# Kernel optimization log

Hardware: AMD Instinct MI355X
Metric: run time of the kernel (lower is better)

Reference implementation:

```python
import jax, jax.numpy as jnp
import numpy as np

B, S, E, D, DV = 4, 4096, 1024, 64, 1024
NEG_INF = jnp.inf


def setup_inputs() -> dict:
    key = jax.random.key(0)
    ks = jax.random.split(key, 5)
    x = jax.random.normal(ks[0], (B, S, E), dtype=jnp.float32)
    Wq = jax.random.normal(ks[1], (E, D), dtype=jnp.float32) * 0.02
    Wk = jax.random.normal(ks[2], (E, D), dtype=jnp.float32) * 0.02
    Wv = jax.random.normal(ks[3], (E, DV), dtype=jnp.float32) * 0.02
    bq = jnp.zeros((D,), dtype=jnp.float32)
    bk = jnp.zeros((D,), dtype=jnp.float32)
    bv = jnp.zeros((DV,), dtype=jnp.float32)
    pad = jax.random.uniform(ks[4], (B, S)) > 0.9
    mask_padding_x = jnp.where(pad, -jnp.inf, 0.0).astype(jnp.float32)
    return {"x": x, "Wq": Wq, "bq": bq, "Wk": Wk, "bk": bk,
            "Wv": Wv, "bv": bv, "mask_padding_x": mask_padding_x}


def _padding_mask(mask_padding_x):
    # Faithful replication of the torch mask-combination logic (self-attn: y mask == x mask).
    mask_x = mask_padding_x[:, :, None]   # [B, Sx, 1]
    mask_y = mask_padding_x[:, None, :]   # [B, 1, Sy]
    # (-inf)*(-inf)=+inf kept; 0*(-inf)=nan -> 0
    prod = jnp.nan_to_num(mask_x * mask_y, nan=0.0, posinf=jnp.inf)
    # one side padded -> -inf; both padded -> inf + (-inf) + (-inf) = nan -> 0; both valid -> 0
    final = jnp.nan_to_num(prod + mask_y + mask_x, nan=0.0, posinf=0.0, neginf=-jnp.inf)
    return final  # [B, Sx, Sy]


def _causal_mask(n):
    # create_mask: strictly-upper-triangular -inf, zeros on/below diagonal
    return jnp.triu(jnp.full((n, n), -jnp.inf, dtype=jnp.float32), k=1)


def reference(x, Wq, bq, Wk, bk, Wv, bv, mask_padding_x):
    # self-attention path (y = x), mask=True (causal), dropout in eval mode (identity)
    Q = jnp.einsum('bse,ed->bsd', x, Wq) + bq          # [B,S,D]
    K = jnp.einsum('bse,ed->bsd', x, Wk) + bk          # [B,S,D]
    V = jnp.einsum('bse,ev->bsv', x, Wv) + bv          # [B,S,DV]
    scale = 1.0 / jnp.sqrt(jnp.float32(D))
    QK = jnp.einsum('bqd,bkd->bqk', Q, K) * scale      # [B,S,S]
    QK = QK + _padding_mask(mask_padding_x)
    QK = QK + _causal_mask(x.shape[1])
    attn = jax.nn.softmax(QK, axis=-1)
    return jnp.einsum('bqk,bkv->bqv', attn, V)         # [B,S,DV]
```

## Files before the change

### kernel.cpp

```cpp
#include <hip/hip_runtime.h>
#include <stdint.h>

typedef __attribute__((ext_vector_type(8))) short short8;
typedef __attribute__((ext_vector_type(4))) float floatx4;

__device__ __forceinline__ unsigned short f2bf(float f) {
    unsigned u = __float_as_uint(f);
    u += 0x7FFFu + ((u >> 16) & 1u);
    return (unsigned short)(u >> 16);
}

__device__ __forceinline__ void gload_lds16(const void* g, void* l) {
    __builtin_amdgcn_global_load_lds(
        (const __attribute__((address_space(1))) unsigned int*)g,
        (__attribute__((address_space(3))) unsigned int*)l, 16, 0, 0);
}

__global__ __launch_bounds__(256)
void conv_x(const float* __restrict__ x, unsigned short* __restrict__ xb) {
    const size_t total = (size_t)16384 * 1024;
    for (size_t i = ((size_t)blockIdx.x * 256 + threadIdx.x) * 8; i < total;
         i += (size_t)2048 * 256 * 8) {
        float4 a = *(const float4*)&x[i];
        float4 b = *(const float4*)&x[i + 4];
        uint4 o;
        o.x = f2bf(a.x) | ((unsigned)f2bf(a.y) << 16);
        o.y = f2bf(a.z) | ((unsigned)f2bf(a.w) << 16);
        o.z = f2bf(b.x) | ((unsigned)f2bf(b.y) << 16);
        o.w = f2bf(b.z) | ((unsigned)f2bf(b.w) << 16);
        *(uint4*)&xb[i] = o;
    }
}

__global__ __launch_bounds__(256)
void transpose_w(const float* __restrict__ src, unsigned short* __restrict__ dst, int N) {
    __shared__ float T[64][65];
    const int t = threadIdx.x;
    const int k0 = blockIdx.x * 64, n0 = blockIdx.y * 64;
    const int r = t >> 4, c4 = (t & 15) * 4;
#pragma unroll
    for (int i = 0; i < 4; i++) {
        float4 v = *(const float4*)&src[(size_t)(k0 + r + 16 * i) * N + n0 + c4];
        T[r + 16 * i][c4] = v.x; T[r + 16 * i][c4 + 1] = v.y;
        T[r + 16 * i][c4 + 2] = v.z; T[r + 16 * i][c4 + 3] = v.w;
    }
    __syncthreads();
#pragma unroll
    for (int i = 0; i < 4; i++) {
        const int n = n0 + r + 16 * i;
        unsigned short b0 = f2bf(T[c4 + 0][r + 16 * i]);
        unsigned short b1 = f2bf(T[c4 + 1][r + 16 * i]);
        unsigned short b2 = f2bf(T[c4 + 2][r + 16 * i]);
        unsigned short b3 = f2bf(T[c4 + 3][r + 16 * i]);
        uint2 pv;
        pv.x = b0 | ((unsigned)b1 << 16);
        pv.y = b2 | ((unsigned)b3 << 16);
        *(uint2*)&dst[(size_t)n * 1024 + k0 + c4] = pv;
    }
}

__global__ __launch_bounds__(128)
void pack_bias(const float* __restrict__ bq, const float* __restrict__ bk,
               float* __restrict__ bqk) {
    const int t = threadIdx.x;
    bqk[t] = (t < 64) ? bq[t] : bk[t - 64];
}

template<bool TRS>
__global__ __launch_bounds__(256)
void gemm_bf16(const unsigned short* __restrict__ A,
               const unsigned short* __restrict__ Bt,
               const float* __restrict__ bias,
               unsigned short* __restrict__ out, int M, int N)
{
    __shared__ unsigned short As[128 * 32];
    __shared__ unsigned short Bs[128 * 32];
    const int tid = threadIdx.x;
    const int w = tid >> 6, l = tid & 63;
    const int quad = l >> 4, l16 = l & 15;
    const int wr = w >> 1, wc = w & 1;
    const int m0 = blockIdx.x * 128, n0 = blockIdx.y * 128;

    const int lr = l >> 2, lk = (l & 3) * 8;
    const unsigned short* Ag0 = A + (size_t)(m0 + w * 16 + lr) * 1024 + lk;
    const unsigned short* Ag1 = Ag0 + (size_t)64 * 1024;
    const unsigned short* Bg0 = Bt + (size_t)(n0 + w * 16 + lr) * 1024 + lk;
    const unsigned short* Bg1 = Bg0 + (size_t)64 * 1024;
    unsigned short* Al0 = &As[w * 512 + l * 8];
    unsigned short* Bl0 = &Bs[w * 512 + l * 8];

    floatx4 acc[4][4];
#pragma unroll
    for (int i = 0; i < 4; i++)
#pragma unroll
        for (int j = 0; j < 4; j++) acc[i][j] = (floatx4)0.f;

    for (int e0 = 0; e0 < 1024; e0 += 32) {
        gload_lds16(Ag0 + e0, Al0);
        gload_lds16(Ag1 + e0, Al0 + 2048);
        gload_lds16(Bg0 + e0, Bl0);
        gload_lds16(Bg1 + e0, Bl0 + 2048);
        __syncthreads();
        short8 af[4], bf[4];
#pragma unroll
        for (int i = 0; i < 4; i++)
            af[i] = *(const short8*)&As[(wr * 64 + i * 16 + l16) * 32 + quad * 8];
#pragma unroll
        for (int j = 0; j < 4; j++)
            bf[j] = *(const short8*)&Bs[(wc * 64 + j * 16 + l16) * 32 + quad * 8];
#pragma unroll
        for (int i = 0; i < 4; i++)
#pragma unroll
            for (int j = 0; j < 4; j++)
                acc[i][j] = __builtin_amdgcn_mfma_f32_16x16x32_bf16(af[i], bf[j], acc[i][j], 0, 0, 0);
        __syncthreads();
    }

#pragma unroll
    for (int j = 0; j < 4; j++) {
        const int n = n0 + wc * 64 + j * 16 + l16;
        const float bn = bias[n];
#pragma unroll
        for (int i = 0; i < 4; i++) {
            const int mb = m0 + wr * 64 + i * 16 + quad * 4;
            if (TRS) {
                unsigned short t[4];
#pragma unroll
                for (int r = 0; r < 4; r++) t[r] = f2bf(acc[i][j][r] + bn);
                uint2 pv;
                pv.x = t[0] | ((unsigned)t[1] << 16);
                pv.y = t[2] | ((unsigned)t[3] << 16);
                *(uint2*)&out[(size_t)n * M + mb] = pv;
            } else {
#pragma unroll
                for (int r = 0; r < 4; r++)
                    out[(size_t)(mb + r) * N + n] = f2bf(acc[i][j][r] + bn);
            }
        }
    }
}

__global__ __launch_bounds__(512, 4)
void attn_fused(const unsigned short* __restrict__ QKb,
                const unsigned short* __restrict__ Vt,
                const float* __restrict__ maskx,
                float* __restrict__ out)
{
    __shared__ unsigned short Qs[64 * 72];
    __shared__ unsigned short Ps[2][64 * 40];
    __shared__ float Ls[64];

    const int tid = threadIdx.x;
    const int wave = tid >> 6, lane = tid & 63;
    const int quad = lane >> 4, l16 = lane & 15;
    const int bid = blockIdx.x;
    const int dvh = bid & 1;
    const int b = (bid >> 1) & 3;
    const int t = bid >> 3;
    const int qt = (t < 32) ? (63 - t) : (t - 32);
    const int q0 = qt * 64;
    const int gq0 = b * 4096 + q0;

    if (tid < 64) Ls[tid] = 0.f;
    {
        const int r = tid >> 3, c = (tid & 7) * 8;
        uint4 v = *(const uint4*)&QKb[(size_t)(gq0 + r) * 128 + c];
        *(uint4*)&Qs[r * 72 + c] = v;
    }
    __syncthreads();

    const int rb = wave >> 1;
    const int kb = wave & 1;
    bool pq[4];
#pragma unroll
    for (int r = 0; r < 4; r++)
        pq[r] = maskx[b * 4096 + q0 + rb * 16 + quad * 4 + r] < -1e30f;

    const short8 qa0 = *(const short8*)&Qs[(rb * 16 + l16) * 72 + quad * 8];
    const short8 qa1 = *(const short8*)&Qs[(rb * 16 + l16) * 72 + 32 + quad * 8];

    floatx4 acc[4][4];
#pragma unroll
    for (int i = 0; i < 4; i++)
#pragma unroll
        for (int j = 0; j < 4; j++) acc[i][j] = (floatx4)0.f;
    float lacc[4] = {0.f, 0.f, 0.f, 0.f};

    const int niter = 2 * qt + 2;
    const float scale = 0.125f;
    const int dv0 = dvh * 512 + wave * 64;

    const unsigned short* kptr = QKb + ((size_t)(b * 4096 + kb * 16 + l16) * 128 + 64 + quad * 8);
    const float* mptr = maskx + b * 4096 + kb * 16 + l16;
    size_t voff[4];
#pragma unroll
    for (int cb = 0; cb < 4; cb++)
        voff[cb] = (size_t)(dv0 + cb * 16 + l16) * 16384 + b * 4096 + quad * 8;

    short8 kc0 = *(const short8*)kptr;
    short8 kc1 = *(const short8*)(kptr + 32);
    float mval = *mptr;

    for (int kt = 0; kt < niter; kt++) {
        const int k0 = kt * 32;
        short8 vb[4];
#pragma unroll
        for (int cb = 0; cb < 4; cb++)
            vb[cb] = *(const short8*)&Vt[voff[cb] + k0];
        floatx4 s = (floatx4)0.f;
        s = __builtin_amdgcn_mfma_f32_16x16x32_bf16(qa0, kc0, s, 0, 0, 0);
        s = __builtin_amdgcn_mfma_f32_16x16x32_bf16(qa1, kc1, s, 0, 0, 0);
        const bool pk = mval < -1e30f;
        {
            int kn = k0 + 32 + kb * 16 + l16;
            if (kn > 4095) kn = 4095;
            const unsigned short* np = QKb + ((size_t)(b * 4096 + kn) * 128 + 64 + quad * 8);
            kc0 = *(const short8*)np;
            kc1 = *(const short8*)(np + 32);
            mval = maskx[b * 4096 + kn];
        }
        const int kg = k0 + kb * 16 + l16;
        unsigned short pbits[4];
#pragma unroll
        for (int r = 0; r < 4; r++) {
            const int qrow = q0 + rb * 16 + quad * 4 + r;
            float p = 0.f;
            if (kg <= qrow && pk == pq[r]) p = __expf(s[r] * scale);
            lacc[r] += p;
            pbits[r] = f2bf(p);
        }
        unsigned short* Pw = Ps[kt & 1];
#pragma unroll
        for (int r = 0; r < 4; r++)
            Pw[(rb * 16 + quad * 4 + r) * 40 + kb * 16 + l16] = pbits[r];
        asm volatile("s_waitcnt lgkmcnt(0)" ::: "memory");
        __builtin_amdgcn_s_barrier();
        __builtin_amdgcn_sched_barrier(0);
        const unsigned short* Pr = Ps[kt & 1];
        short8 pa[4];
#pragma unroll
        for (int r2 = 0; r2 < 4; r2++)
            pa[r2] = *(const short8*)&Pr[(r2 * 16 + l16) * 40 + quad * 8];
#pragma unroll
        for (int cb = 0; cb < 4; cb++)
#pragma unroll
            for (int r2 = 0; r2 < 4; r2++)
                acc[r2][cb] = __builtin_amdgcn_mfma_f32_16x16x32_bf16(pa[r2], vb[cb], acc[r2][cb], 0, 0, 0);
    }

#pragma unroll
    for (int r = 0; r < 4; r++) {
        float v = lacc[r];
        v += __shfl_xor(v, 1);
        v += __shfl_xor(v, 2);
        v += __shfl_xor(v, 4);
        v += __shfl_xor(v, 8);
        if (l16 == 0) atomicAdd(&Ls[rb * 16 + quad * 4 + r], v);
    }
    __syncthreads();

#pragma unroll
    for (int r2 = 0; r2 < 4; r2++) {
#pragma unroll
        for (int r = 0; r < 4; r++) {
            const int qrow = q0 + r2 * 16 + quad * 4 + r;
            const float inv = 1.f / Ls[r2 * 16 + quad * 4 + r];
#pragma unroll
            for (int cb = 0; cb < 4; cb++)
                out[(size_t)(b * 4096 + qrow) * 1024 + dv0 + cb * 16 + l16] = acc[r2][cb][r] * inv;
        }
    }
}

extern "C" void kernel_launch(void* const* d_in, const int* in_sizes, int n_in,
                              void* d_out, int out_size, void* d_ws, size_t ws_size,
                              hipStream_t stream) {
    const float* x  = (const float*)d_in[0];
    const float* Wq = (const float*)d_in[1];
    const float* bq = (const float*)d_in[2];
    const float* Wk = (const float*)d_in[3];
    const float* bk = (const float*)d_in[4];
    const float* Wv = (const float*)d_in[5];
    const float* bv = (const float*)d_in[6];
    const float* mk = (const float*)d_in[7];
    float* out = (float*)d_out;

    const int M = 4 * 4096;
    char* ws = (char*)d_ws;
    unsigned short* Xb   = (unsigned short*)ws;
    unsigned short* Vt   = (unsigned short*)(ws + (33554432));
    unsigned short* Wvt  = (unsigned short*)(ws + (67108864));
    unsigned short* Wqkt = (unsigned short*)(ws + (69206016));
    unsigned short* QKb  = (unsigned short*)(ws + (69468160));
    float*          bqk  = (float*)(ws + (73662464));

    conv_x<<<2048, 256, 0, stream>>>(x, Xb);
    transpose_w<<<dim3(16, 16), 256, 0, stream>>>(Wv, Wvt, 1024);
    transpose_w<<<dim3(16, 1), 256, 0, stream>>>(Wq, Wqkt, 64);
    transpose_w<<<dim3(16, 1), 256, 0, stream>>>(Wk, Wqkt + 64 * 1024, 64);
    pack_bias<<<1, 128, 0, stream>>>(bq, bk, bqk);

    gemm_bf16<true ><<<dim3(128, 8), 256, 0, stream>>>(Xb, Wvt, bv, Vt, M, 1024);
    gemm_bf16<false><<<dim3(128, 1), 256, 0, stream>>>(Xb, Wqkt, bqk, QKb, M, 128);

    attn_fused<<<dim3(4 * 64 * 2), 512, 0, stream>>>(QKb, Vt, mk, out);
}
```

Measured before the change: 417.3 us.

## Split attention work into 256-thread blocks over eight DV slices

The fused attention kernel now uses 256-thread blocks, each covering 128 of the 1024 value columns instead of 512, so the grid grows from 512 to 2048 blocks. Each wave now computes scores for two 16-row query slabs and accumulates two 16-column value tiles instead of four. This gives more, smaller blocks for load balancing and occupancy across CUs. The cost is that QK^T scores and the exp/softmax numerators are recomputed four times as often, once per DV slice.

```diff
diff --git a/kernel.cpp b/kernel.cpp
--- a/kernel.cpp
+++ b/kernel.cpp
@@ -140,7 +140,7 @@
     }
 }
 
-__global__ __launch_bounds__(512, 4)
+__global__ __launch_bounds__(256, 4)
 void attn_fused(const unsigned short* __restrict__ QKb,
                 const unsigned short* __restrict__ Vt,
                 const float* __restrict__ maskx,
@@ -154,63 +154,80 @@
     const int wave = tid >> 6, lane = tid & 63;
     const int quad = lane >> 4, l16 = lane & 15;
     const int bid = blockIdx.x;
-    const int dvh = bid & 1;
+    const int dvl = bid & 1;
     const int b = (bid >> 1) & 3;
-    const int t = bid >> 3;
+    const int dvh2 = (bid >> 3) & 3;
+    const int t = bid >> 5;
+    const int dvq = dvh2 * 2 + dvl;
     const int qt = (t < 32) ? (63 - t) : (t - 32);
     const int q0 = qt * 64;
     const int gq0 = b * 4096 + q0;
 
     if (tid < 64) Ls[tid] = 0.f;
     {
-        const int r = tid >> 3, c = (tid & 7) * 8;
-        uint4 v = *(const uint4*)&QKb[(size_t)(gq0 + r) * 128 + c];
-        *(uint4*)&Qs[r * 72 + c] = v;
+#pragma unroll
+        for (int j = 0; j < 2; j++) {
+            const int c = tid + j * 256;
+            const int r = c >> 3, c8 = (c & 7) * 8;
+            uint4 v = *(const uint4*)&QKb[(size_t)(gq0 + r) * 128 + c8];
+            *(uint4*)&Qs[r * 72 + c8] = v;
+        }
     }
     __syncthreads();
 
-    const int rb = wave >> 1;
+    const int rbp = wave >> 1;
     const int kb = wave & 1;
-    bool pq[4];
-#pragma unroll
-    for (int r = 0; r < 4; r++)
-        pq[r] = maskx[b * 4096 + q0 + rb * 16 + quad * 4 + r] < -1e30f;
-
-    const short8 qa0 = *(const short8*)&Qs[(rb * 16 + l16) * 72 + quad * 8];
-    const short8 qa1 = *(const short8*)&Qs[(rb * 16 + l16) * 72 + 32 + quad * 8];
-
-    floatx4 acc[4][4];
+
+    unsigned pqm = 0;
+#pragma unroll
+    for (int h = 0; h < 2; h++)
+#pragma unroll
+        for (int r = 0; r < 4; r++)
+            if (maskx[b * 4096 + q0 + (rbp * 2 + h) * 16 + quad * 4 + r] < -1e30f)
+                pqm |= 1u << (h * 4 + r);
+
+    short8 qa[2][2];
+#pragma unroll
+    for (int h = 0; h < 2; h++) {
+        qa[h][0] = *(const short8*)&Qs[((rbp * 2 + h) * 16 + l16) * 72 + quad * 8];
+        qa[h][1] = *(const short8*)&Qs[((rbp * 2 + h) * 16 + l16) * 72 + 32 + quad * 8];
+    }
+
+    floatx4 acc[4][2];
 #pragma unroll
     for (int i = 0; i < 4; i++)
 #pragma unroll
-        for (int j = 0; j < 4; j++) acc[i][j] = (floatx4)0.f;
-    float lacc[4] = {0.f, 0.f, 0.f, 0.f};
+        for (int j = 0; j < 2; j++) acc[i][j] = (floatx4)0.f;
+    float lacc[2][4] = {{0.f, 0.f, 0.f, 0.f}, {0.f, 0.f, 0.f, 0.f}};
 
     const int niter = 2 * qt + 2;
     const float scale = 0.125f;
-    const int dv0 = dvh * 512 + wave * 64;
+    const int dv0 = dvq * 128 + wave * 32;
 
     const unsigned short* kptr = QKb + ((size_t)(b * 4096 + kb * 16 + l16) * 128 + 64 + quad * 8);
-    const float* mptr = maskx + b * 4096 + kb * 16 + l16;
-    size_t voff[4];
-#pragma unroll
-    for (int cb = 0; cb < 4; cb++)
+    size_t voff[2];
+#pragma unroll
+    for (int cb = 0; cb < 2; cb++)
         voff[cb] = (size_t)(dv0 + cb * 16 + l16) * 16384 + b * 4096 + quad * 8;
 
     short8 kc0 = *(const short8*)kptr;
     short8 kc1 = *(const short8*)(kptr + 32);
-    float mval = *mptr;
+    float mval = maskx[b * 4096 + kb * 16 + l16];
 
     for (int kt = 0; kt < niter; kt++) {
         const int k0 = kt * 32;
-        short8 vb[4];
-#pragma unroll
-        for (int cb = 0; cb < 4; cb++)
+        short8 vb[2];
+#pragma unroll
+        for (int cb = 0; cb < 2; cb++)
             vb[cb] = *(const short8*)&Vt[voff[cb] + k0];
-        floatx4 s = (floatx4)0.f;
-        s = __builtin_amdgcn_mfma_f32_16x16x32_bf16(qa0, kc0, s, 0, 0, 0);
-        s = __builtin_amdgcn_mfma_f32_16x16x32_bf16(qa1, kc1, s, 0, 0, 0);
-        const bool pk = mval < -1e30f;
+        floatx4 s[2];
+#pragma unroll
+        for (int h = 0; h < 2; h++) {
+            s[h] = (floatx4)0.f;
+            s[h] = __builtin_amdgcn_mfma_f32_16x16x32_bf16(qa[h][0], kc0, s[h], 0, 0, 0);
+            s[h] = __builtin_amdgcn_mfma_f32_16x16x32_bf16(qa[h][1], kc1, s[h], 0, 0, 0);
+        }
+        const unsigned pkb = (mval < -1e30f) ? 1u : 0u;
         {
             int kn = k0 + 32 + kb * 16 + l16;
             if (kn > 4095) kn = 4095;
@@ -220,19 +237,19 @@
             mval = maskx[b * 4096 + kn];
         }
         const int kg = k0 + kb * 16 + l16;
-        unsigned short pbits[4];
-#pragma unroll
-        for (int r = 0; r < 4; r++) {
-            const int qrow = q0 + rb * 16 + quad * 4 + r;
-            float p = 0.f;
-            if (kg <= qrow && pk == pq[r]) p = __expf(s[r] * scale);
-            lacc[r] += p;
-            pbits[r] = f2bf(p);
-        }
         unsigned short* Pw = Ps[kt & 1];
 #pragma unroll
-        for (int r = 0; r < 4; r++)
-            Pw[(rb * 16 + quad * 4 + r) * 40 + kb * 16 + l16] = pbits[r];
+        for (int h = 0; h < 2; h++) {
+#pragma unroll
+            for (int r = 0; r < 4; r++) {
+                const int qrow = q0 + (rbp * 2 + h) * 16 + quad * 4 + r;
+                float p = 0.f;
+                if (kg <= qrow && ((pqm >> (h * 4 + r)) & 1u) == pkb)
+                    p = __expf(s[h][r] * scale);
+                lacc[h][r] += p;
+                Pw[((rbp * 2 + h) * 16 + quad * 4 + r) * 40 + kb * 16 + l16] = f2bf(p);
+            }
+        }
         asm volatile("s_waitcnt lgkmcnt(0)" ::: "memory");
         __builtin_amdgcn_s_barrier();
         __builtin_amdgcn_sched_barrier(0);
@@ -242,21 +259,23 @@
         for (int r2 = 0; r2 < 4; r2++)
             pa[r2] = *(const short8*)&Pr[(r2 * 16 + l16) * 40 + quad * 8];
 #pragma unroll
-        for (int cb = 0; cb < 4; cb++)
+        for (int cb = 0; cb < 2; cb++)
 #pragma unroll
             for (int r2 = 0; r2 < 4; r2++)
                 acc[r2][cb] = __builtin_amdgcn_mfma_f32_16x16x32_bf16(pa[r2], vb[cb], acc[r2][cb], 0, 0, 0);
     }
 
 #pragma unroll
-    for (int r = 0; r < 4; r++) {
-        float v = lacc[r];
-        v += __shfl_xor(v, 1);
-        v += __shfl_xor(v, 2);
-        v += __shfl_xor(v, 4);
-        v += __shfl_xor(v, 8);
-        if (l16 == 0) atomicAdd(&Ls[rb * 16 + quad * 4 + r], v);
-    }
+    for (int h = 0; h < 2; h++)
+#pragma unroll
+        for (int r = 0; r < 4; r++) {
+            float v = lacc[h][r];
+            v += __shfl_xor(v, 1);
+            v += __shfl_xor(v, 2);
+            v += __shfl_xor(v, 4);
+            v += __shfl_xor(v, 8);
+            if (l16 == 0) atomicAdd(&Ls[(rbp * 2 + h) * 16 + quad * 4 + r], v);
+        }
     __syncthreads();
 
 #pragma unroll
@@ -266,7 +285,7 @@
             const int qrow = q0 + r2 * 16 + quad * 4 + r;
             const float inv = 1.f / Ls[r2 * 16 + quad * 4 + r];
 #pragma unroll
-            for (int cb = 0; cb < 4; cb++)
+            for (int cb = 0; cb < 2; cb++)
                 out[(size_t)(b * 4096 + qrow) * 1024 + dv0 + cb * 16 + l16] = acc[r2][cb][r] * inv;
         }
     }
@@ -303,5 +322,5 @@
     gemm_bf16<true ><<<dim3(128, 8), 256, 0, stream>>>(Xb, Wvt, bv, Vt, M, 1024);
     gemm_bf16<false><<<dim3(128, 1), 256, 0, stream>>>(Xb, Wqkt, bqk, QKb, M, 128);
 
-    attn_fused<<<dim3(4 * 64 * 2), 512, 0, stream>>>(QKb, Vt, mk, out);
-}
+    attn_fused<<<dim3(4 * 64 * 8), 256, 0, stream>>>(QKb, Vt, mk, out);
+}
```

Result: slower. 482.1 us (+15.5%).
